# Optimization experiments

Measured on AMD Instinct MI355X. Metric: run time of the kernel, lower is better.

## Reference

```python
import jax
import jax.numpy as jnp
import numpy as np

IN_FEATS = 784
HIDDEN_DIM = 1024
BATCH = 1024


def setup_inputs() -> dict:
    key = jax.random.key(0)
    k_px, k_W, k_c, k_V, k_b = jax.random.split(key, 5)
    pixels = jax.random.uniform(k_px, (BATCH, IN_FEATS), dtype=jnp.float32)
    W = jax.random.normal(k_W, (HIDDEN_DIM, IN_FEATS), dtype=jnp.float32)
    c = jax.random.normal(k_c, (HIDDEN_DIM,), dtype=jnp.float32)
    V = jax.random.normal(k_V, (IN_FEATS, HIDDEN_DIM), dtype=jnp.float32)
    b = jax.random.normal(k_b, (IN_FEATS,), dtype=jnp.float32)
    return {"pixels": pixels, "W": W, "c": c, "V": V, "b": b}


def reference(pixels, W, c, V, b):
    # pixels: [B, D]; W: [H, D]; c: [H]; V: [D, H]; b: [D]
    B = pixels.shape[0]
    a0 = jnp.broadcast_to(c[None, :], (B, c.shape[0]))  # [B, H]

    def step(a, inp):
        w_col, v_row, b_i, x_i = inp  # [H], [H], [], [B]
        h = jax.nn.sigmoid(a)                     # [B, H]
        pred_i = b_i + h @ v_row                  # [B]
        a_next = a + w_col[None, :] * x_i[:, None]  # rank-1 accumulator update
        return a_next, pred_i

    xs = (W.T, V, b, pixels.T)  # each leading dim D (scan over visible units)
    _, preds = jax.lax.scan(step, a0, xs)  # preds: [D, B]
    return preds.T  # [B, D]
```

## Files before the change

kernel.cpp:

```cpp
#include <hip/hip_runtime.h>
#include <stdint.h>

#define B_ 1024
#define D_ 784
#define H_ 1024
#define BH_ (B_ * H_)
#define LOG2E 1.4426950408889634f


__device__ __forceinline__ unsigned short bf16_rne(float x) {
    unsigned b = __float_as_uint(x);
    return (unsigned short)((b + 0x7FFFu + ((b >> 16) & 1u)) >> 16);
}

__device__ __forceinline__ int seg_bound(int s) {
    const int b[5] = {0, 200, 392, 592, 784};
    return b[s];
}

__global__ __launch_bounds__(256) void prep(const float* __restrict__ V,
                                            const float* __restrict__ W,
                                            const float* __restrict__ px,
                                            unsigned short* __restrict__ VWb,
                                            float* __restrict__ G) {
    __shared__ float smem[1056];
    const int t = threadIdx.x;

    if (blockIdx.x < 800) {
        int i0 = (blockIdx.x % 25) * 32;
        int h0 = (blockIdx.x / 25) * 32;
        int tx = t & 31, ty = t >> 5;
        int hb = h0 >> 8, hr = h0 & 255;
#pragma unroll
        for (int j = 0; j < 4; ++j) {
            int i = i0 + ty + j * 8;
            if (i < D_)
                VWb[((size_t)i * 4 + hb) * 512 + hr + tx] = bf16_rne(V[(size_t)i * H_ + h0 + tx]);
        }
#pragma unroll
        for (int j = 0; j < 4; ++j) {
            int h = h0 + ty + j * 8;
            int i = i0 + tx;
            float v = 0.f;
            if (i < D_) v = W[(size_t)h * D_ + i] * LOG2E;
            smem[(ty + j * 8) * 33 + tx] = v;
        }
        __syncthreads();
#pragma unroll
        for (int j = 0; j < 4; ++j) {
            int i = i0 + ty + j * 8;
            if (i < D_)
                VWb[((size_t)i * 4 + hb) * 512 + 256 + hr + tx] = bf16_rne(smem[tx * 33 + ty + j * 8]);
        }
    } else {
        float* xs = smem;
        float* ws = smem + 512;
        int idx = blockIdx.x - 800;
        int r   = idx >> 8;
        int b0  = (idx & 15) * 64;
        int h0  = ((idx >> 4) & 15) * 64;
        int j0s = seg_bound(r), j1s = seg_bound(r + 1);

        const int tb = t >> 4, th = t & 15;
        float acc[4][4];
#pragma unroll
        for (int bi = 0; bi < 4; ++bi)
#pragma unroll
            for (int hh = 0; hh < 4; ++hh) acc[bi][hh] = 0.f;

        const int xb = t >> 3;
        const int xj = t & 7;
        const int wh = t >> 1, wj = (t & 1) * 4;

        for (int j0 = j0s; j0 < j1s; j0 += 8) {
            float xv0 = px[(size_t)(b0 + xb) * D_ + j0 + xj];
            float xv1 = px[(size_t)(b0 + 32 + xb) * D_ + j0 + xj];
            float4 wv = make_float4(0, 0, 0, 0);
            if (t < 128) wv = *(const float4*)(W + (size_t)(h0 + wh) * D_ + j0 + wj);
            __syncthreads();
            xs[xj * 64 + xb]      = xv0;
            xs[xj * 64 + 32 + xb] = xv1;
            if (t < 128) {
                ws[(wj + 0) * 64 + wh] = wv.x * LOG2E;
                ws[(wj + 1) * 64 + wh] = wv.y * LOG2E;
                ws[(wj + 2) * 64 + wh] = wv.z * LOG2E;
                ws[(wj + 3) * 64 + wh] = wv.w * LOG2E;
            }
            __syncthreads();
#pragma unroll
            for (int jj = 0; jj < 8; ++jj) {
                float4 xq = *(float4*)&xs[jj * 64 + tb * 4];
                float4 wq = *(float4*)&ws[jj * 64 + th * 4];
                float xa[4] = {xq.x, xq.y, xq.z, xq.w};
                float wa[4] = {wq.x, wq.y, wq.z, wq.w};
#pragma unroll
                for (int bi = 0; bi < 4; ++bi)
#pragma unroll
                    for (int hh = 0; hh < 4; ++hh)
                        acc[bi][hh] = fmaf(xa[bi], wa[hh], acc[bi][hh]);
            }
        }
        float* dst = G + (size_t)r * BH_;
#pragma unroll
        for (int bi = 0; bi < 4; ++bi) {
            float4 o = make_float4(acc[bi][0], acc[bi][1], acc[bi][2], acc[bi][3]);
            *(float4*)(dst + (size_t)(b0 + tb * 4 + bi) * H_ + h0 + th * 4) = o;
        }
    }
}

template <int CTRL>
__device__ __forceinline__ float dpp_add(float p) {
    int s = __builtin_amdgcn_update_dpp(0, __float_as_int(p), CTRL, 0xf, 0xf, true);
    return p + __int_as_float(s);
}
__device__ __forceinline__ float reduce_halves(float p) {
    p = dpp_add<0x111>(p);
    p = dpp_add<0x112>(p);
    p = dpp_add<0x114>(p);
    p = dpp_add<0x118>(p);
    p = dpp_add<0x142>(p);
    return p;
}

__device__ __forceinline__ void cvt8(uint4 u, float4& a, float4& b) {
    a.x = __uint_as_float(u.x << 16);
    a.y = __uint_as_float(u.x);
    a.z = __uint_as_float(u.y << 16);
    a.w = __uint_as_float(u.y);
    b.x = __uint_as_float(u.z << 16);
    b.y = __uint_as_float(u.z);
    b.z = __uint_as_float(u.w << 16);
    b.w = __uint_as_float(u.w);
}

__global__ __launch_bounds__(256, 8) void nade_main(
    const float* __restrict__ px,
    const float* __restrict__ c,
    const unsigned short* __restrict__ VWb,
    const float* __restrict__ G,
    const float* __restrict__ bias,
    float* __restrict__ out)
{
    __shared__ float4 red[2][4][2];

    const int lane = threadIdx.x & 63;
    const int wid  = threadIdx.x >> 6;
    const int bid  = blockIdx.x;
    const int s    = bid >> 9;
    const int rp   = bid & 511;
    const int half = lane >> 5;
    const int row  = rp * 2 + half;
    const int hl   = lane & 31;
    const int h0   = wid * 256 + hl * 8;

    const int i0s = seg_bound(s), i1s = seg_bound(s + 1);

    float A[8];
    {
        float4 c0 = *(const float4*)(c + h0);
        float4 c1 = *(const float4*)(c + h0 + 4);
        A[0] = c0.x * LOG2E; A[1] = c0.y * LOG2E; A[2] = c0.z * LOG2E; A[3] = c0.w * LOG2E;
        A[4] = c1.x * LOG2E; A[5] = c1.y * LOG2E; A[6] = c1.z * LOG2E; A[7] = c1.w * LOG2E;
        for (int r = 0; r < s; ++r) {
            const float* gp = G + (size_t)r * BH_ + (size_t)row * H_ + h0;
            float4 g0 = *(const float4*)(gp);
            float4 g1 = *(const float4*)(gp + 4);
            A[0] += g0.x; A[1] += g0.y; A[2] += g0.z; A[3] += g0.w;
            A[4] += g1.x; A[5] += g1.y; A[6] += g1.z; A[7] += g1.w;
        }
    }

    const float* xp = px + (size_t)row * D_;
    const uint4* vw = (const uint4*)VWb + ((size_t)i0s * 4 + wid) * 64 + hl;

    auto step8 = [&A](const float4& v0, const float4& v1,
                      const float4& w0, const float4& w1, float xi) -> float {
        float va[8] = {v0.x, v0.y, v0.z, v0.w, v1.x, v1.y, v1.z, v1.w};
        float wa[8] = {w0.x, w0.y, w0.z, w0.w, w1.x, w1.y, w1.z, w1.w};
        float q[8];
#pragma unroll
        for (int k = 0; k < 8; ++k) {
            float e = __builtin_amdgcn_exp2f(fminf(15.f, -A[k]));
            q[k] = 1.f + e;
            A[k] = fmaf(wa[k], xi, A[k]);
        }
        float a01 = fmaf(va[0], q[1], va[1] * q[0]);
        float a23 = fmaf(va[2], q[3], va[3] * q[2]);
        float a45 = fmaf(va[4], q[5], va[5] * q[4]);
        float a67 = fmaf(va[6], q[7], va[7] * q[6]);
        float q01 = q[0] * q[1], q23 = q[2] * q[3];
        float q45 = q[4] * q[5], q67 = q[6] * q[7];
        float n0123 = fmaf(a01, q23, a23 * q01);
        float n4567 = fmaf(a45, q67, a67 * q45);
        float q0123 = q01 * q23, q4567 = q45 * q67;
        float r = __builtin_amdgcn_rcpf(q0123 * q4567);
        float n = fmaf(n0123, q4567, n4567 * q0123);
        return n * r;
    };

    uint4 uv = vw[0], uw = vw[32];
    vw += 256;
    float4 xq = *(const float4*)(xp + i0s);

    for (int ib = i0s; ib < i1s; ib += 4) {
        int xb = (ib + 4 < i1s) ? (ib + 4) : i0s;
        float4 xq_n = *(const float4*)(xp + xb);
        float xa[4] = {xq.x, xq.y, xq.z, xq.w};
        float pr[4];
#pragma unroll
        for (int j = 0; j < 4; ++j) {
            uint4 uvn = vw[0], uwn = vw[32];
            vw += 256;
            float4 v0, v1, w0, w1;
            cvt8(uv, v0, v1);
            cvt8(uw, w0, w1);
            float p = step8(v0, v1, w0, w1, xa[j]);
            pr[j] = reduce_halves(p);
            uv = uvn; uw = uwn;
        }
        const int par = (ib >> 2) & 1;
        if (hl == 31) red[par][wid][half] = make_float4(pr[0], pr[1], pr[2], pr[3]);
        __syncthreads();
        if (threadIdx.x < 2) {
            float4 b4 = *(const float4*)(bias + ib);
            float4 p0 = red[par][0][threadIdx.x];
            float4 p1 = red[par][1][threadIdx.x];
            float4 p2 = red[par][2][threadIdx.x];
            float4 p3 = red[par][3][threadIdx.x];
            float4 o;
            o.x = b4.x + ((p0.x + p1.x) + (p2.x + p3.x));
            o.y = b4.y + ((p0.y + p1.y) + (p2.y + p3.y));
            o.z = b4.z + ((p0.z + p1.z) + (p2.z + p3.z));
            o.w = b4.w + ((p0.w + p1.w) + (p2.w + p3.w));
            *(float4*)(out + (size_t)(rp * 2 + threadIdx.x) * D_ + ib) = o;
        }
        xq = xq_n;
    }
}

extern "C" void kernel_launch(void* const* d_in, const int* in_sizes, int n_in,
                              void* d_out, int out_size, void* d_ws, size_t ws_size,
                              hipStream_t stream) {
    const float* px   = (const float*)d_in[0];
    const float* W    = (const float*)d_in[1];
    const float* c    = (const float*)d_in[2];
    const float* V    = (const float*)d_in[3];
    const float* bias = (const float*)d_in[4];
    float* out = (float*)d_out;

    unsigned short* VWb = (unsigned short*)d_ws;
    float* G    = (float*)((char*)d_ws + (size_t)788 * 4096);

    prep<<<dim3(1568), 256, 0, stream>>>(V, W, px, VWb, G);

    nade_main<<<dim3(2048), 256, 0, stream>>>(px, c, VWb, G, bias, out);
}
```

Before: 299.5 us.

## Assign one batch row per wavefront to drop shared-memory reduction and barrier

Restructures nade_main so each wavefront owns a whole batch row and processes two 8-wide hidden chunks per lane (16 hidden units). The per-step dot product is now reduced entirely within the wave using a full 64-lane DPP reduction, which removes the shared-memory staging and the __syncthreads per group of four steps. The grid is halved and launch bounds lowered to 4 blocks/CU. In exchange each thread holds twice the accumulator state and loads, raising register pressure and reducing the number of resident waves available to hide latency.

```diff
diff --git a/kernel.cpp b/kernel.cpp
--- a/kernel.cpp
+++ b/kernel.cpp
@@ -114,12 +114,13 @@
     int s = __builtin_amdgcn_update_dpp(0, __float_as_int(p), CTRL, 0xf, 0xf, true);
     return p + __int_as_float(s);
 }
-__device__ __forceinline__ float reduce_halves(float p) {
+__device__ __forceinline__ float reduce64(float p) {
     p = dpp_add<0x111>(p);
     p = dpp_add<0x112>(p);
     p = dpp_add<0x114>(p);
     p = dpp_add<0x118>(p);
     p = dpp_add<0x142>(p);
+    p = dpp_add<0x143>(p);
     return p;
 }
 
@@ -134,7 +135,34 @@
     b.w = __uint_as_float(u.w);
 }
 
-__global__ __launch_bounds__(256, 8) void nade_main(
+__device__ __forceinline__ void tree8(float (&Aq)[8], const uint4& uv, const uint4& uw,
+                                      float xi, float& n, float& d) {
+    float4 v0, v1, w0, w1;
+    cvt8(uv, v0, v1);
+    cvt8(uw, w0, w1);
+    float va[8] = {v0.x, v0.y, v0.z, v0.w, v1.x, v1.y, v1.z, v1.w};
+    float wa[8] = {w0.x, w0.y, w0.z, w0.w, w1.x, w1.y, w1.z, w1.w};
+    float q[8];
+#pragma unroll
+    for (int k = 0; k < 8; ++k) {
+        float e = __builtin_amdgcn_exp2f(fminf(15.f, -Aq[k]));
+        q[k] = 1.f + e;
+        Aq[k] = fmaf(wa[k], xi, Aq[k]);
+    }
+    float a01 = fmaf(va[0], q[1], va[1] * q[0]);
+    float a23 = fmaf(va[2], q[3], va[3] * q[2]);
+    float a45 = fmaf(va[4], q[5], va[5] * q[4]);
+    float a67 = fmaf(va[6], q[7], va[7] * q[6]);
+    float q01 = q[0] * q[1], q23 = q[2] * q[3];
+    float q45 = q[4] * q[5], q67 = q[6] * q[7];
+    float n0123 = fmaf(a01, q23, a23 * q01);
+    float n4567 = fmaf(a45, q67, a67 * q45);
+    float q0123 = q01 * q23, q4567 = q45 * q67;
+    d = q0123 * q4567;
+    n = fmaf(n0123, q4567, n4567 * q0123);
+}
+
+__global__ __launch_bounds__(256, 4) void nade_main(
     const float* __restrict__ px,
     const float* __restrict__ c,
     const unsigned short* __restrict__ VWb,
@@ -142,64 +170,45 @@
     const float* __restrict__ bias,
     float* __restrict__ out)
 {
-    __shared__ float4 red[2][4][2];
-
     const int lane = threadIdx.x & 63;
     const int wid  = threadIdx.x >> 6;
     const int bid  = blockIdx.x;
-    const int s    = bid >> 9;
-    const int rp   = bid & 511;
-    const int half = lane >> 5;
-    const int row  = rp * 2 + half;
-    const int hl   = lane & 31;
-    const int h0   = wid * 256 + hl * 8;
+    const int s    = bid >> 8;
+    const int rb   = bid & 255;
+    const int row  = rb * 4 + wid;
 
     const int i0s = seg_bound(s), i1s = seg_bound(s + 1);
 
-    float A[8];
+    const int hA = lane * 8;
+    const int hB = 512 + hA;
+
+    float AA[8], AB[8];
     {
-        float4 c0 = *(const float4*)(c + h0);
-        float4 c1 = *(const float4*)(c + h0 + 4);
-        A[0] = c0.x * LOG2E; A[1] = c0.y * LOG2E; A[2] = c0.z * LOG2E; A[3] = c0.w * LOG2E;
-        A[4] = c1.x * LOG2E; A[5] = c1.y * LOG2E; A[6] = c1.z * LOG2E; A[7] = c1.w * LOG2E;
+        float4 c0 = *(const float4*)(c + hA);
+        float4 c1 = *(const float4*)(c + hA + 4);
+        float4 c2 = *(const float4*)(c + hB);
+        float4 c3 = *(const float4*)(c + hB + 4);
+        AA[0] = c0.x * LOG2E; AA[1] = c0.y * LOG2E; AA[2] = c0.z * LOG2E; AA[3] = c0.w * LOG2E;
+        AA[4] = c1.x * LOG2E; AA[5] = c1.y * LOG2E; AA[6] = c1.z * LOG2E; AA[7] = c1.w * LOG2E;
+        AB[0] = c2.x * LOG2E; AB[1] = c2.y * LOG2E; AB[2] = c2.z * LOG2E; AB[3] = c2.w * LOG2E;
+        AB[4] = c3.x * LOG2E; AB[5] = c3.y * LOG2E; AB[6] = c3.z * LOG2E; AB[7] = c3.w * LOG2E;
         for (int r = 0; r < s; ++r) {
-            const float* gp = G + (size_t)r * BH_ + (size_t)row * H_ + h0;
-            float4 g0 = *(const float4*)(gp);
-            float4 g1 = *(const float4*)(gp + 4);
-            A[0] += g0.x; A[1] += g0.y; A[2] += g0.z; A[3] += g0.w;
-            A[4] += g1.x; A[5] += g1.y; A[6] += g1.z; A[7] += g1.w;
+            const float* gp = G + (size_t)r * BH_ + (size_t)row * H_;
+            float4 g0 = *(const float4*)(gp + hA);
+            float4 g1 = *(const float4*)(gp + hA + 4);
+            float4 g2 = *(const float4*)(gp + hB);
+            float4 g3 = *(const float4*)(gp + hB + 4);
+            AA[0] += g0.x; AA[1] += g0.y; AA[2] += g0.z; AA[3] += g0.w;
+            AA[4] += g1.x; AA[5] += g1.y; AA[6] += g1.z; AA[7] += g1.w;
+            AB[0] += g2.x; AB[1] += g2.y; AB[2] += g2.z; AB[3] += g2.w;
+            AB[4] += g3.x; AB[5] += g3.y; AB[6] += g3.z; AB[7] += g3.w;
         }
     }
 
     const float* xp = px + (size_t)row * D_;
-    const uint4* vw = (const uint4*)VWb + ((size_t)i0s * 4 + wid) * 64 + hl;
-
-    auto step8 = [&A](const float4& v0, const float4& v1,
-                      const float4& w0, const float4& w1, float xi) -> float {
-        float va[8] = {v0.x, v0.y, v0.z, v0.w, v1.x, v1.y, v1.z, v1.w};
-        float wa[8] = {w0.x, w0.y, w0.z, w0.w, w1.x, w1.y, w1.z, w1.w};
-        float q[8];
-#pragma unroll
-        for (int k = 0; k < 8; ++k) {
-            float e = __builtin_amdgcn_exp2f(fminf(15.f, -A[k]));
-            q[k] = 1.f + e;
-            A[k] = fmaf(wa[k], xi, A[k]);
-        }
-        float a01 = fmaf(va[0], q[1], va[1] * q[0]);
-        float a23 = fmaf(va[2], q[3], va[3] * q[2]);
-        float a45 = fmaf(va[4], q[5], va[5] * q[4]);
-        float a67 = fmaf(va[6], q[7], va[7] * q[6]);
-        float q01 = q[0] * q[1], q23 = q[2] * q[3];
-        float q45 = q[4] * q[5], q67 = q[6] * q[7];
-        float n0123 = fmaf(a01, q23, a23 * q01);
-        float n4567 = fmaf(a45, q67, a67 * q45);
-        float q0123 = q01 * q23, q4567 = q45 * q67;
-        float r = __builtin_amdgcn_rcpf(q0123 * q4567);
-        float n = fmaf(n0123, q4567, n4567 * q0123);
-        return n * r;
-    };
-
-    uint4 uv = vw[0], uw = vw[32];
+    const uint4* vw = (const uint4*)VWb + (size_t)i0s * 256 + (lane >> 5) * 64 + (lane & 31);
+
+    uint4 vA = vw[0], wA = vw[32], vB = vw[128], wB = vw[160];
     vw += 256;
     float4 xq = *(const float4*)(xp + i0s);
 
@@ -210,30 +219,20 @@
         float pr[4];
 #pragma unroll
         for (int j = 0; j < 4; ++j) {
-            uint4 uvn = vw[0], uwn = vw[32];
+            uint4 vAn = vw[0], wAn = vw[32], vBn = vw[128], wBn = vw[160];
             vw += 256;
-            float4 v0, v1, w0, w1;
-            cvt8(uv, v0, v1);
-            cvt8(uw, w0, w1);
-            float p = step8(v0, v1, w0, w1, xa[j]);
-            pr[j] = reduce_halves(p);
-            uv = uvn; uw = uwn;
-        }
-        const int par = (ib >> 2) & 1;
-        if (hl == 31) red[par][wid][half] = make_float4(pr[0], pr[1], pr[2], pr[3]);
-        __syncthreads();
-        if (threadIdx.x < 2) {
-            float4 b4 = *(const float4*)(bias + ib);
-            float4 p0 = red[par][0][threadIdx.x];
-            float4 p1 = red[par][1][threadIdx.x];
-            float4 p2 = red[par][2][threadIdx.x];
-            float4 p3 = red[par][3][threadIdx.x];
-            float4 o;
-            o.x = b4.x + ((p0.x + p1.x) + (p2.x + p3.x));
-            o.y = b4.y + ((p0.y + p1.y) + (p2.y + p3.y));
-            o.z = b4.z + ((p0.z + p1.z) + (p2.z + p3.z));
-            o.w = b4.w + ((p0.w + p1.w) + (p2.w + p3.w));
-            *(float4*)(out + (size_t)(rp * 2 + threadIdx.x) * D_ + ib) = o;
+            float nA, dA, nB, dB;
+            tree8(AA, vA, wA, xa[j], nA, dA);
+            tree8(AB, vB, wB, xa[j], nB, dB);
+            float p = fmaf(nA, __builtin_amdgcn_rcpf(dA),
+                           nB * __builtin_amdgcn_rcpf(dB));
+            pr[j] = reduce64(p);
+            vA = vAn; wA = wAn; vB = vBn; wB = wBn;
+        }
+        float4 b4 = *(const float4*)(bias + ib);
+        if (lane == 63) {
+            float4 o = make_float4(pr[0] + b4.x, pr[1] + b4.y, pr[2] + b4.z, pr[3] + b4.w);
+            *(float4*)(out + (size_t)row * D_ + ib) = o;
         }
         xq = xq_n;
     }
@@ -254,5 +253,5 @@
 
     prep<<<dim3(1568), 256, 0, stream>>>(V, W, px, VWb, G);
 
-    nade_main<<<dim3(2048), 256, 0, stream>>>(px, c, VWb, G, bias, out);
-}
+    nade_main<<<dim3(1024), 256, 0, stream>>>(px, c, VWb, G, bias, out);
+}
```

Result: slower. 314.1 us (+4.9%).
